# Kernel optimization log

Hardware: AMD Instinct MI355X
Metric: run time of the kernel (lower is better)

Reference implementation:

```python
import jax, jax.numpy as jnp
import numpy as np

B, S, IN, N, MOT = 128, 4096, 6, 64, 3
ODE_UNFOLDS = 6
EPS = 1e-8


def setup_inputs() -> dict:
    ks = jax.random.split(jax.random.key(0), 20)
    u = lambda k, shape, lo, hi: jax.random.uniform(k, shape, jnp.float32, lo, hi)
    pm1 = lambda k, shape: jnp.where(jax.random.bernoulli(k, 0.5, shape), 1.0, -1.0).astype(jnp.float32)
    return {
        "x": jax.random.normal(ks[0], (B, S, IN), jnp.float32),
        "mean_us": 0.1 * jax.random.normal(ks[1], (IN,), jnp.float32),
        "std_us": u(ks[2], (IN,), 0.5, 1.5),
        "input_w": u(ks[3], (IN,), 0.8, 1.2),
        "input_b": 0.01 * jax.random.normal(ks[4], (IN,), jnp.float32),
        "output_w": u(ks[5], (MOT,), 0.8, 1.2),
        "output_b": 0.01 * jax.random.normal(ks[6], (MOT,), jnp.float32),
        "gleak": u(ks[7], (N,), 0.001, 1.0),
        "vleak": u(ks[8], (N,), -0.2, 0.2),
        "cm": u(ks[9], (N,), 0.4, 0.6),
        "sensory_W": u(ks[10], (IN, N), 0.001, 1.0),
        "sensory_mu": u(ks[11], (IN, N), 0.3, 0.8),
        "sensory_sigma": u(ks[12], (IN, N), 3.0, 8.0),
        "sensory_erev": pm1(ks[13], (IN, N)),
        "W": u(ks[14], (N, N), 0.001, 1.0),
        "mu": u(ks[15], (N, N), 0.3, 0.8),
        "sigma": u(ks[16], (N, N), 3.0, 8.0),
        "erev": pm1(ks[17], (N, N)),
    }


def _ltc_sequence(x, mean_us, std_us, input_w, input_b, output_w, output_b,
                  gleak, vleak, cm, sensory_W, sensory_mu, sensory_sigma,
                  sensory_erev, W, mu, sigma, erev):
    # normalize inputs (DgaRawSequence) then LTCCell input mapping
    xn = (x - mean_us) / std_us                      # [B,S,IN]
    xm = xn * input_w + input_b                      # [B,S,IN]
    cm_t = cm * ODE_UNFOLDS                          # cm / (elapsed_time=1 / ode_unfolds)

    def step(v, u_t):                                # v: [B,N], u_t: [B,IN]
        # sensory synapse activations [B,IN,N]
        s_act = sensory_W * jax.nn.sigmoid((u_t[:, :, None] - sensory_mu) * sensory_sigma)
        wns = jnp.sum(s_act * sensory_erev, axis=1)  # [B,N]
        wds = jnp.sum(s_act, axis=1)                 # [B,N]
        for _ in range(ODE_UNFOLDS):
            w_act = W * jax.nn.sigmoid((v[:, :, None] - mu) * sigma)  # [B,N,N]
            num = cm_t * v + gleak * vleak + jnp.sum(w_act * erev, axis=1) + wns
            den = cm_t + gleak + jnp.sum(w_act, axis=1) + wds
            v = num / (den + EPS)
        return v, v

    v0 = jnp.zeros((x.shape[0], gleak.shape[0]), dtype=x.dtype)
    _, vs = jax.lax.scan(step, v0, jnp.swapaxes(xm, 0, 1))   # [S,B,N]
    states = jnp.swapaxes(vs, 0, 1)                          # [B,S,N]
    # LTCCell output mapping (motor neurons = first MOT states)
    out = states[..., :MOT] * output_w + output_b            # [B,S,3]
    # denormalize (DgaRawSequence)
    return out * std_us[:MOT] + mean_us[:MOT]


def reference(x, mean_us, std_us, input_w, input_b, output_w, output_b,
              gleak, vleak, cm, sensory_W, sensory_mu, sensory_sigma,
              sensory_erev, W, mu, sigma, erev):
    return _ltc_sequence(x, mean_us, std_us, input_w, input_b, output_w,
                         output_b, gleak, vleak, cm, sensory_W, sensory_mu,
                         sensory_sigma, sensory_erev, W, mu, sigma, erev)
```

## Files before the change

### kernel.cpp

```cpp
#include <hip/hip_runtime.h>

#define B_ 128
#define S_ 4096
#define IN_ 6
#define N_ 64
#define MOT_ 3
#define UNF 6
#define EPS_ 1e-8f
#define LOG2E 1.4426950408889634f

__device__ __forceinline__ float red8(float x) {
    int r = __builtin_amdgcn_update_dpp(0, __float_as_int(x), 0x128 ,
                                        0xF, 0xF, true);
    return x + __int_as_float(r);
}
__device__ __forceinline__ float red16(float x) {
#if __has_builtin(__builtin_amdgcn_permlane16_swap)
    auto r = __builtin_amdgcn_permlane16_swap(__float_as_int(x), __float_as_int(x),
                                              false, false);
    return __int_as_float((int)r[0]) + __int_as_float((int)r[1]);
#else
    return x + __shfl_xor(x, 16, 64);
#endif
}
__device__ __forceinline__ float red32(float x) {
#if __has_builtin(__builtin_amdgcn_permlane32_swap)
    auto r = __builtin_amdgcn_permlane32_swap(__float_as_int(x), __float_as_int(x),
                                              false, false);
    return __int_as_float((int)r[0]) + __int_as_float((int)r[1]);
#else
    return x + __shfl_xor(x, 32, 64);
#endif
}

__device__ __forceinline__ void lds_barrier() {
    asm volatile("s_waitcnt lgkmcnt(0)" ::: "memory");
    __builtin_amdgcn_s_barrier();
}

__launch_bounds__(512, 1)
__global__ void ltc_kernel(
    const float* __restrict__ x,
    const float* __restrict__ mean_us, const float* __restrict__ std_us,
    const float* __restrict__ input_w, const float* __restrict__ input_b,
    const float* __restrict__ output_w, const float* __restrict__ output_b,
    const float* __restrict__ gleak, const float* __restrict__ vleak,
    const float* __restrict__ cm,
    const float* __restrict__ sW, const float* __restrict__ sMu,
    const float* __restrict__ sSig, const float* __restrict__ sErev,
    const float* __restrict__ W, const float* __restrict__ Mu,
    const float* __restrict__ Sig, const float* __restrict__ Erev,
    float* __restrict__ out)
{
    const int b    = blockIdx.x;
    const int t    = threadIdx.x;
    const int lane = t & 63;
    const int w    = t >> 6;
    const int cc   = lane >> 3;
    const int ii   = lane & 7;
    const int myCol = w * 8 + ii;
    const int jb   = cc * 8;

    __shared__ __align__(16) float vbuf[2][N_];
    __shared__ float s_lds[IN_][N_][2];

    float A[8], Bc[8], Wr[8], We[8];
#pragma unroll
    for (int jj = 0; jj < 8; ++jj) {
        int idx = (jb + jj) * N_ + myCol;
        float sg = Sig[idx], m = Mu[idx], ww = W[idx], e = Erev[idx];
        A[jj]  = -sg * LOG2E;
        Bc[jj] = m * sg * LOG2E;
        Wr[jj] = ww;
        We[jj] = ww * e;
    }

    const float cmt = cm[myCol] * (float)UNF;
    const float glk = gleak[myCol];
    const float gv  = glk * vleak[myCol];
    const float dbase = cmt + glk + EPS_;

    float SA = 0.f, SB = 0.f, SWv = 0.f, SWe = 0.f, nscale = 0.f, nbias = 0.f;
    if (w < IN_) {
        int idx = w * N_ + lane;
        float sg = sSig[idx], m = sMu[idx], ww = sW[idx], e = sErev[idx];
        SA  = -sg * LOG2E;
        SB  = m * sg * LOG2E;
        SWv = ww;
        SWe = ww * e;
        nscale = input_w[w] / std_us[w];
        nbias  = input_b[w] - mean_us[w] / std_us[w] * input_w[w];
    }

    float OW = 0.f, OB = 0.f;
    if (t < MOT_) {
        OW = output_w[t] * std_us[t];
        OB = output_b[t] * std_us[t] + mean_us[t];
    }

    const float* xb = x + (size_t)b * S_ * IN_;
    float* ob = out + (size_t)b * S_ * MOT_;

    if (t < N_) vbuf[0][t] = 0.f;
    if (w < IN_) {
        float u  = fmaf(xb[w], nscale, nbias);
        float e  = __builtin_amdgcn_exp2f(fmaf(u, SA, SB));
        float sg = __builtin_amdgcn_rcpf(1.0f + e);
        s_lds[w][lane][0] = SWe * sg;
        s_lds[w][lane][1] = SWv * sg;
    }
    lds_barrier();

    float v_my = 0.f;

    for (int s = 0; s < S_; ++s) {
        float xnext = 0.f;
        if (w < IN_) xnext = xb[((s + 1 < S_) ? (s + 1) : s) * IN_ + w];

        float a = 0.f, d = 0.f;
#pragma unroll
        for (int ci = 0; ci < IN_; ++ci) {
            float2 sv = *(const float2*)&s_lds[ci][myCol][0];
            a += sv.x; d += sv.y;
        }
        const float nb = gv + a;
        const float db = dbase + d;

#pragma unroll
        for (int k = 0; k < UNF; ++k) {
            const int p = k & 1;
            float4 va = *(const float4*)&vbuf[p][jb];
            float4 vc = *(const float4*)&vbuf[p][jb + 4];
            const float vj[8] = {va.x, va.y, va.z, va.w, vc.x, vc.y, vc.z, vc.w};

            float pn = 0.f, pd = 0.f;
#pragma unroll
            for (int jj = 0; jj < 8; ++jj) {
                float e  = __builtin_amdgcn_exp2f(fmaf(vj[jj], A[jj], Bc[jj]));
                float sg = __builtin_amdgcn_rcpf(1.0f + e);
                pn = fmaf(We[jj], sg, pn);
                pd = fmaf(Wr[jj], sg, pd);
            }
            pn = red8(pn);   pd = red8(pd);
            pn = red16(pn);  pd = red16(pd);
            pn = red32(pn);  pd = red32(pd);

            float num = fmaf(cmt, v_my, nb + pn);
            v_my = num * __builtin_amdgcn_rcpf(db + pd);

            if (cc == 0) vbuf[p ^ 1][myCol] = v_my;

            if (k == 1 && w < IN_) {
                float u  = fmaf(xnext, nscale, nbias);
                float e2 = __builtin_amdgcn_exp2f(fmaf(u, SA, SB));
                float sg = __builtin_amdgcn_rcpf(1.0f + e2);
                s_lds[w][lane][0] = SWe * sg;
                s_lds[w][lane][1] = SWv * sg;
            }
            lds_barrier();
        }

        if (t < MOT_) ob[s * MOT_ + t] = fmaf(v_my, OW, OB);
    }
}

extern "C" void kernel_launch(void* const* d_in, const int* in_sizes, int n_in,
                              void* d_out, int out_size, void* d_ws, size_t ws_size,
                              hipStream_t stream) {
    (void)in_sizes; (void)n_in; (void)d_ws; (void)ws_size; (void)out_size;
    const float* x       = (const float*)d_in[0];
    const float* mean_us = (const float*)d_in[1];
    const float* std_us  = (const float*)d_in[2];
    const float* input_w = (const float*)d_in[3];
    const float* input_b = (const float*)d_in[4];
    const float* out_w   = (const float*)d_in[5];
    const float* out_b   = (const float*)d_in[6];
    const float* gleak   = (const float*)d_in[7];
    const float* vleak   = (const float*)d_in[8];
    const float* cm      = (const float*)d_in[9];
    const float* sW      = (const float*)d_in[10];
    const float* sMu     = (const float*)d_in[11];
    const float* sSig    = (const float*)d_in[12];
    const float* sErev   = (const float*)d_in[13];
    const float* W       = (const float*)d_in[14];
    const float* Mu      = (const float*)d_in[15];
    const float* Sig     = (const float*)d_in[16];
    const float* Erev    = (const float*)d_in[17];
    float* out = (float*)d_out;

    ltc_kernel<<<dim3(B_), dim3(512), 0, stream>>>(
        x, mean_us, std_us, input_w, input_b, out_w, out_b,
        gleak, vleak, cm, sW, sMu, sSig, sErev, W, Mu, Sig, Erev, out);
}
```

Baseline: 10.41 ms.

## Halve block to 256 threads, compute sensory terms per thread, use packed FMA

Reassigns work so each lane handles 16 presynaptic neurons instead of 8, halving the block to 4 waves. This drops the DPP 8-lane reduction step and lowers the number of waves meeting at each barrier. The sensory synapse sums, previously built by dedicated waves and passed through LDS, are now recomputed redundantly in every thread straight from registers, with x for the next step prefetched as float2 loads. The inner sigmoid uses 2-wide vector FMA. In exchange, each lane carries a longer serial exp/rcp chain per unfold, plus extra sensory work per step.

```diff
diff --git a/kernel.cpp b/kernel.cpp
--- a/kernel.cpp
+++ b/kernel.cpp
@@ -9,11 +9,8 @@
 #define EPS_ 1e-8f
 #define LOG2E 1.4426950408889634f
 
-__device__ __forceinline__ float red8(float x) {
-    int r = __builtin_amdgcn_update_dpp(0, __float_as_int(x), 0x128 ,
-                                        0xF, 0xF, true);
-    return x + __int_as_float(r);
-}
+typedef float v2f __attribute__((ext_vector_type(2)));
+
 __device__ __forceinline__ float red16(float x) {
 #if __has_builtin(__builtin_amdgcn_permlane16_swap)
     auto r = __builtin_amdgcn_permlane16_swap(__float_as_int(x), __float_as_int(x),
@@ -38,7 +35,7 @@
     __builtin_amdgcn_s_barrier();
 }
 
-__launch_bounds__(512, 1)
+__launch_bounds__(256, 1)
 __global__ void ltc_kernel(
     const float* __restrict__ x,
     const float* __restrict__ mean_us, const float* __restrict__ std_us,
@@ -56,21 +53,21 @@
     const int t    = threadIdx.x;
     const int lane = t & 63;
     const int w    = t >> 6;
-    const int cc   = lane >> 3;
-    const int ii   = lane & 7;
-    const int myCol = w * 8 + ii;
-    const int jb   = cc * 8;
+    const int cc   = lane >> 4;
+    const int ii   = lane & 15;
+    const int myCol = w * 16 + ii;
+    const int jb   = cc * 16;
 
     __shared__ __align__(16) float vbuf[2][N_];
-    __shared__ float s_lds[IN_][N_][2];
-
-    float A[8], Bc[8], Wr[8], We[8];
-#pragma unroll
-    for (int jj = 0; jj < 8; ++jj) {
+
+    v2f A2[8], B2[8];
+    float Wr[16], We[16];
+#pragma unroll
+    for (int jj = 0; jj < 16; ++jj) {
         int idx = (jb + jj) * N_ + myCol;
         float sg = Sig[idx], m = Mu[idx], ww = W[idx], e = Erev[idx];
-        A[jj]  = -sg * LOG2E;
-        Bc[jj] = m * sg * LOG2E;
+        A2[jj >> 1][jj & 1] = -sg * LOG2E;
+        B2[jj >> 1][jj & 1] = m * sg * LOG2E;
         Wr[jj] = ww;
         We[jj] = ww * e;
     }
@@ -80,16 +77,17 @@
     const float gv  = glk * vleak[myCol];
     const float dbase = cmt + glk + EPS_;
 
-    float SA = 0.f, SB = 0.f, SWv = 0.f, SWe = 0.f, nscale = 0.f, nbias = 0.f;
-    if (w < IN_) {
-        int idx = w * N_ + lane;
+    float SA[IN_], SB[IN_], SWe[IN_], SWv[IN_], NS[IN_], NB[IN_];
+#pragma unroll
+    for (int ci = 0; ci < IN_; ++ci) {
+        int idx = ci * N_ + myCol;
         float sg = sSig[idx], m = sMu[idx], ww = sW[idx], e = sErev[idx];
-        SA  = -sg * LOG2E;
-        SB  = m * sg * LOG2E;
-        SWv = ww;
-        SWe = ww * e;
-        nscale = input_w[w] / std_us[w];
-        nbias  = input_b[w] - mean_us[w] / std_us[w] * input_w[w];
+        SA[ci]  = -sg * LOG2E;
+        SB[ci]  = m * sg * LOG2E;
+        SWv[ci] = ww;
+        SWe[ci] = ww * e;
+        NS[ci]  = input_w[ci] / std_us[ci];
+        NB[ci]  = input_b[ci] - mean_us[ci] / std_us[ci] * input_w[ci];
     }
 
     float OW = 0.f, OB = 0.f;
@@ -102,64 +100,80 @@
     float* ob = out + (size_t)b * S_ * MOT_;
 
     if (t < N_) vbuf[0][t] = 0.f;
-    if (w < IN_) {
-        float u  = fmaf(xb[w], nscale, nbias);
-        float e  = __builtin_amdgcn_exp2f(fmaf(u, SA, SB));
-        float sg = __builtin_amdgcn_rcpf(1.0f + e);
-        s_lds[w][lane][0] = SWe * sg;
-        s_lds[w][lane][1] = SWv * sg;
-    }
-    lds_barrier();
+
+    float xc[IN_];
+    {
+        int off = 0;
+        asm volatile("" : "+v"(off));
+        float2 x01 = *(const float2*)(xb + off);
+        float2 x23 = *(const float2*)(xb + off + 2);
+        float2 x45 = *(const float2*)(xb + off + 4);
+        xc[0] = x01.x; xc[1] = x01.y; xc[2] = x23.x;
+        xc[3] = x23.y; xc[4] = x45.x; xc[5] = x45.y;
+    }
+    __syncthreads();
 
     float v_my = 0.f;
 
     for (int s = 0; s < S_; ++s) {
-        float xnext = 0.f;
-        if (w < IN_) xnext = xb[((s + 1 < S_) ? (s + 1) : s) * IN_ + w];
-
-        float a = 0.f, d = 0.f;
+        const int s1 = (s + 1 < S_) ? (s + 1) : s;
+        int off = s1 * IN_;
+        asm volatile("" : "+v"(off));
+        float2 p01 = *(const float2*)(xb + off);
+        float2 p23 = *(const float2*)(xb + off + 2);
+        float2 p45 = *(const float2*)(xb + off + 4);
+
+        float wns = 0.f, wds = 0.f;
 #pragma unroll
         for (int ci = 0; ci < IN_; ++ci) {
-            float2 sv = *(const float2*)&s_lds[ci][myCol][0];
-            a += sv.x; d += sv.y;
+            float u  = fmaf(xc[ci], NS[ci], NB[ci]);
+            float e  = __builtin_amdgcn_exp2f(fmaf(u, SA[ci], SB[ci]));
+            float sg = __builtin_amdgcn_rcpf(1.0f + e);
+            wns = fmaf(SWe[ci], sg, wns);
+            wds = fmaf(SWv[ci], sg, wds);
         }
-        const float nb = gv + a;
-        const float db = dbase + d;
+        const float nbs = gv + wns;
+        const float dbs = dbase + wds;
 
 #pragma unroll
         for (int k = 0; k < UNF; ++k) {
             const int p = k & 1;
-            float4 va = *(const float4*)&vbuf[p][jb];
-            float4 vc = *(const float4*)&vbuf[p][jb + 4];
-            const float vj[8] = {va.x, va.y, va.z, va.w, vc.x, vc.y, vc.z, vc.w};
-
-            float pn = 0.f, pd = 0.f;
-#pragma unroll
-            for (int jj = 0; jj < 8; ++jj) {
-                float e  = __builtin_amdgcn_exp2f(fmaf(vj[jj], A[jj], Bc[jj]));
-                float sg = __builtin_amdgcn_rcpf(1.0f + e);
-                pn = fmaf(We[jj], sg, pn);
-                pd = fmaf(Wr[jj], sg, pd);
+            float4 q0 = *(const float4*)&vbuf[p][jb];
+            float4 q1 = *(const float4*)&vbuf[p][jb + 4];
+            float4 q2 = *(const float4*)&vbuf[p][jb + 8];
+            float4 q3 = *(const float4*)&vbuf[p][jb + 12];
+            const v2f vp[8] = {
+                {q0.x, q0.y}, {q0.z, q0.w}, {q1.x, q1.y}, {q1.z, q1.w},
+                {q2.x, q2.y}, {q2.z, q2.w}, {q3.x, q3.y}, {q3.z, q3.w}};
+
+            float pn0 = 0.f, pd0 = 0.f, pn1 = 0.f, pd1 = 0.f;
+#pragma unroll
+            for (int pi = 0; pi < 8; ++pi) {
+                v2f z  = __builtin_elementwise_fma(vp[pi], A2[pi], B2[pi]);
+                v2f e  = {__builtin_amdgcn_exp2f(z.x), __builtin_amdgcn_exp2f(z.y)};
+                v2f tt = e + 1.0f;
+                float s0 = __builtin_amdgcn_rcpf(tt.x);
+                float s1x = __builtin_amdgcn_rcpf(tt.y);
+                pn0 = fmaf(We[2*pi],   s0,  pn0);
+                pd0 = fmaf(Wr[2*pi],   s0,  pd0);
+                pn1 = fmaf(We[2*pi+1], s1x, pn1);
+                pd1 = fmaf(Wr[2*pi+1], s1x, pd1);
             }
-            pn = red8(pn);   pd = red8(pd);
+            float pn = pn0 + pn1;
+            float pd = pd0 + pd1;
+
             pn = red16(pn);  pd = red16(pd);
             pn = red32(pn);  pd = red32(pd);
 
-            float num = fmaf(cmt, v_my, nb + pn);
-            v_my = num * __builtin_amdgcn_rcpf(db + pd);
-
-            if (cc == 0) vbuf[p ^ 1][myCol] = v_my;
-
-            if (k == 1 && w < IN_) {
-                float u  = fmaf(xnext, nscale, nbias);
-                float e2 = __builtin_amdgcn_exp2f(fmaf(u, SA, SB));
-                float sg = __builtin_amdgcn_rcpf(1.0f + e2);
-                s_lds[w][lane][0] = SWe * sg;
-                s_lds[w][lane][1] = SWv * sg;
-            }
+            v_my = fmaf(cmt, v_my, nbs + pn) * __builtin_amdgcn_rcpf(dbs + pd);
+
+            if (lane < 16) vbuf[p ^ 1][w * 16 + lane] = v_my;
+
             lds_barrier();
         }
 
+        xc[0] = p01.x; xc[1] = p01.y; xc[2] = p23.x;
+        xc[3] = p23.y; xc[4] = p45.x; xc[5] = p45.y;
         if (t < MOT_) ob[s * MOT_ + t] = fmaf(v_my, OW, OB);
     }
 }
@@ -188,7 +202,7 @@
     const float* Erev    = (const float*)d_in[17];
     float* out = (float*)d_out;
 
-    ltc_kernel<<<dim3(B_), dim3(512), 0, stream>>>(
+    ltc_kernel<<<dim3(B_), dim3(256), 0, stream>>>(
         x, mean_us, std_us, input_w, input_b, out_w, out_b,
         gleak, vleak, cm, sW, sMu, sSig, sErev, W, Mu, Sig, Erev, out);
 }
```

Measured after the change: 9.187 ms. 11.7% less time.
